# Kernel tuning notes

Hardware: AMD Instinct MI355X
Metric: run time of the kernel (lower is better)

Reference implementation:

```python
import jax, jax.numpy as jnp
import numpy as np

N_NODES = 50000
N_EDGES = 800000
IN_F = 256
OUT_F = 64
N_HEADS = 8
LRELU_SLOPE = 0.2


def setup_inputs() -> dict:
    key = jax.random.key(0)
    ks = jax.random.split(key, 6)
    x = jax.random.normal(ks[0], (N_NODES, IN_F), dtype=jnp.float32)
    src = jax.random.randint(ks[1], (N_EDGES,), 0, N_NODES, dtype=jnp.int32)
    dst = jax.random.randint(ks[2], (N_EDGES,), 0, N_NODES, dtype=jnp.int32)
    M_values = jax.random.uniform(ks[3], (N_EDGES,), dtype=jnp.float32)
    # xavier_uniform-ish scale (gain=1.414)
    wscale = 1.414 * np.sqrt(6.0 / (IN_F + OUT_F))
    W = jax.random.uniform(ks[4], (N_HEADS, IN_F, OUT_F), dtype=jnp.float32,
                           minval=-wscale, maxval=wscale)
    ascale = 1.414 * np.sqrt(6.0 / (OUT_F + 1))
    a = jax.random.uniform(ks[5], (N_HEADS, 2, OUT_F), dtype=jnp.float32,
                           minval=-ascale, maxval=ascale)
    return {"x": x, "src": src, "dst": dst, "M_values": M_values, "W": W, "a": a}


def reference(x, src, dst, M_values, W, a):
    # x: [N, Fin]; src/dst: [E]; M_values: [E] (edge-aligned mask/weights)
    # W: [H, Fin, Fout]; a: [H, 2, Fout] (a[:,0]=a_self, a[:,1]=a_neighs)
    N = x.shape[0]
    outs = []
    for hidx in range(W.shape[0]):  # small fixed head count
        h = x @ W[hidx]                       # [N, Fout]
        a_self = h @ a[hidx, 0]               # [N]
        a_neigh = h @ a[hidx, 1]              # [N]
        e = jax.nn.leaky_relu(a_self[src] + a_neigh[dst], LRELU_SLOPE) * M_values  # [E]
        exp_e = jnp.exp(e)
        denom = jax.ops.segment_sum(exp_e, dst, num_segments=N)   # [N]
        att = exp_e / (denom[dst] + 1e-16)                        # [E]
        h_prime = jax.ops.segment_sum(att[:, None] * h[src], dst, num_segments=N)  # [N, Fout]
        outs.append(jax.nn.elu(h_prime))      # concat=True -> elu per head
    return jnp.concatenate(outs, axis=1)       # [N, H*Fout]
```

## Files before the change

### kernel.cpp

```cpp
#include <hip/hip_runtime.h>
#include <math.h>

#define N_NODES 50000
#define N_EDGES 800000
#define IN_F 256
#define OUT_F 64
#define N_HEADS 8
#define SLOPE 0.2f

typedef __attribute__((ext_vector_type(8))) __bf16 bf16x8;
typedef __attribute__((ext_vector_type(4))) __bf16 bf16x4;
typedef __attribute__((ext_vector_type(4))) float floatx4;
typedef __attribute__((ext_vector_type(4))) float f32x4;
typedef __attribute__((ext_vector_type(2))) int i32x2;
typedef __attribute__((ext_vector_type(8))) char schar8;

#define HIST_BLOCKS   3125
#define CAST_W_BLOCKS 512
#define PREP_BLOCKS   (HIST_BLOCKS + CAST_W_BLOCKS)

__global__ __launch_bounds__(256) void prep_kernel(const float* __restrict__ W,
                                                   const int* __restrict__ dst,
                                                   __bf16* __restrict__ Wt,
                                                   int* __restrict__ deg) {
    const int b = blockIdx.x;
    const int t = threadIdx.x;
    if (b < HIST_BLOCKS) {
        int e = b * 256 + t;
        atomicAdd(&deg[dst[e]], 1);
    } else {
        int i = (b - HIST_BLOCKS) * 256 + t;
        int n = i & (OUT_F - 1);
        int k = (i >> 6) & (IN_F - 1);
        int h = i >> 14;
        Wt[((size_t)h * OUT_F + n) * IN_F + k] = (__bf16)W[i];
    }
}

#define XPAD 264
__global__ __launch_bounds__(256) void mfma_gemm_kernel(const float* __restrict__ x,
                                                        const __bf16* __restrict__ Wt,
                                                        const float* __restrict__ a,
                                                        signed char* __restrict__ hb,
                                                        float2* __restrict__ asc,
                                                        float* __restrict__ a_neigh) {
    __shared__ __bf16 xs[32][XPAD];
    const int warp = threadIdx.x >> 6;
    const int tile = blockIdx.x;
    const int n0 = tile * 32;
    const int lane = threadIdx.x & 63;
    const int l15 = lane & 15;
    const int quad = lane >> 4;
    const int h0 = warp * 2;

#pragma unroll
    for (int i = 0; i < 8; i++) {
        int c4 = i * 256 + threadIdx.x;
        int row = c4 >> 6;
        int col = (c4 & 63) * 4;
        int node = n0 + row;
        node = (node < N_NODES) ? node : (N_NODES - 1);
        f32x4 v = __builtin_nontemporal_load((const f32x4*)x + (size_t)node * 64 + (c4 & 63));
        bf16x4 o;
        o[0] = (__bf16)v[0]; o[1] = (__bf16)v[1]; o[2] = (__bf16)v[2]; o[3] = (__bf16)v[3];
        *(bf16x4*)&xs[row][col] = o;
    }
    __syncthreads();

    floatx4 acc[2][2][4];
#pragma unroll
    for (int hh = 0; hh < 2; hh++)
#pragma unroll
        for (int i = 0; i < 2; i++)
#pragma unroll
            for (int c = 0; c < 4; c++) acc[hh][i][c] = floatx4{0.f, 0.f, 0.f, 0.f};

    const __bf16* wb0 = Wt + ((size_t)h0 * OUT_F + l15) * IN_F + quad * 8;
    const __bf16* wb1 = wb0 + (size_t)OUT_F * IN_F;

#pragma unroll
    for (int k0 = 0; k0 < IN_F; k0 += 32) {
        bf16x8 a0 = *(const bf16x8*)&xs[l15][k0 + quad * 8];
        bf16x8 a1 = *(const bf16x8*)&xs[l15 + 16][k0 + quad * 8];
#pragma unroll
        for (int c = 0; c < 4; c++) {
            bf16x8 b0 = *(const bf16x8*)(wb0 + (size_t)c * 16 * IN_F + k0);
            acc[0][0][c] = __builtin_amdgcn_mfma_f32_16x16x32_bf16(a0, b0, acc[0][0][c], 0, 0, 0);
            acc[0][1][c] = __builtin_amdgcn_mfma_f32_16x16x32_bf16(a1, b0, acc[0][1][c], 0, 0, 0);
            bf16x8 b1 = *(const bf16x8*)(wb1 + (size_t)c * 16 * IN_F + k0);
            acc[1][0][c] = __builtin_amdgcn_mfma_f32_16x16x32_bf16(a0, b1, acc[1][0][c], 0, 0, 0);
            acc[1][1][c] = __builtin_amdgcn_mfma_f32_16x16x32_bf16(a1, b1, acc[1][1][c], 0, 0, 0);
        }
    }

    __syncthreads();
    char* myc = (char*)xs + warp * (32 * OUT_F);

#pragma unroll
    for (int hh = 0; hh < 2; hh++) {
        const int head = h0 + hh;
        float av0[4], av1[4];
#pragma unroll
        for (int c = 0; c < 4; c++) {
            av0[c] = a[head * 2 * OUT_F + c * 16 + l15];
            av1[c] = a[head * 2 * OUT_F + OUT_F + c * 16 + l15];
        }
#pragma unroll
        for (int i = 0; i < 2; i++) {
#pragma unroll
            for (int reg = 0; reg < 4; reg++) {
                float ps = 0.f, pn = 0.f, rm = 0.f;
#pragma unroll
                for (int c = 0; c < 4; c++) {
                    float v = acc[hh][i][c][reg];
                    ps = fmaf(v, av0[c], ps);
                    pn = fmaf(v, av1[c], pn);
                    rm = fmaxf(rm, fabsf(v));
                }
#pragma unroll
                for (int off = 1; off < 16; off <<= 1) {
                    ps += __shfl_xor(ps, off, 64);
                    pn += __shfl_xor(pn, off, 64);
                    rm = fmaxf(rm, __shfl_xor(rm, off, 64));
                }
                const float inv = (rm > 0.f) ? 127.f / rm : 0.f;
                const int rowoff = (i * 16 + quad * 4 + reg) * OUT_F;
#pragma unroll
                for (int c = 0; c < 4; c++) {
                    float q = rintf(acc[hh][i][c][reg] * inv);
                    q = fminf(fmaxf(q, -127.f), 127.f);
                    myc[rowoff + c * 16 + l15] = (char)(int)q;
                }
                int node = n0 + i * 16 + quad * 4 + reg;
                if (l15 == 0 && node < N_NODES) {
                    asc[node * N_HEADS + head] = make_float2(ps, rm * (1.f / 127.f));
                    a_neigh[node * N_HEADS + head] = pn;
                }
            }
        }
#pragma unroll
        for (int pass = 0; pass < 4; pass++) {
            int row = pass * 8 + (lane >> 3);
            int node = n0 + row;
            schar8 v = *(const schar8*)&myc[row * OUT_F + (lane & 7) * 8];
            if (node < N_NODES)
                *(schar8*)(hb + ((size_t)(node * N_HEADS + head) << 6) + (lane & 7) * 8) = v;
        }
    }
}

#define SB 512
#define NSB 98
__global__ void scanA(const int* __restrict__ deg, int* __restrict__ start,
                      int* __restrict__ bsum) {
    __shared__ int tmp[SB];
    int t = threadIdx.x, i = blockIdx.x * SB + t;
    int v = (i < N_NODES) ? deg[i] : 0;
    tmp[t] = v;
    for (int off = 1; off < SB; off <<= 1) {
        __syncthreads();
        int add = (t >= off) ? tmp[t - off] : 0;
        __syncthreads();
        tmp[t] += add;
    }
    if (i < N_NODES) start[i] = tmp[t] - v;
    if (t == SB - 1) bsum[blockIdx.x] = tmp[SB - 1];
}

__global__ void scanC(int* __restrict__ start, const int* __restrict__ bsum,
                      int* __restrict__ cursor) {
    __shared__ int pre[128];
    int t = threadIdx.x;
    if (t < 128) pre[t] = (t < NSB) ? bsum[t] : 0;
    __syncthreads();
    for (int off = 1; off < 128; off <<= 1) {
        int add = (t < 128 && t >= off) ? pre[t - off] : 0;
        __syncthreads();
        if (t < 128) pre[t] += add;
        __syncthreads();
    }
    int excl = (blockIdx.x == 0) ? 0 : pre[blockIdx.x - 1];
    int i = blockIdx.x * SB + t;
    if (i < N_NODES) {
        int s = start[i] + excl;
        start[i] = s;
        cursor[i] = s;
    }
}

__global__ void fill_kernel(const int* __restrict__ src, const int* __restrict__ dst,
                            const float* __restrict__ M, int* __restrict__ cursor,
                            i32x2* __restrict__ csr_sm) {
    int e = blockIdx.x * 256 + threadIdx.x;
    if (e < N_EDGES) {
        int d = dst[e];
        int pos = atomicAdd(&cursor[d], 1);
        i32x2 v;
        v.x = src[e];
        v.y = __float_as_int(M[e]);
        __builtin_nontemporal_store(v, csr_sm + pos);
    }
}

__global__ __launch_bounds__(256) void agg_kernel(const signed char* __restrict__ hb,
                                                  const float2* __restrict__ asc,
                                                  const float* __restrict__ a_neigh,
                                                  const int* __restrict__ start,
                                                  const int* __restrict__ deg,
                                                  const i32x2* __restrict__ csr_sm,
                                                  float* __restrict__ out) {
    int n = blockIdx.x * 4 + (threadIdx.x >> 6);
    if (n >= N_NODES) return;
    const int lane = threadIdx.x & 63;
    const int head = lane >> 3;

    const int d = deg[n];
    const float an = a_neigh[(n << 3) + head];
    const signed char* hbl = hb + (lane << 3);
    const float2* aslc = asc + head;
    const i32x2* cp = csr_sm + start[n];

    float facc[8];
#pragma unroll
    for (int k = 0; k < 8; k++) facc[k] = 0.f;
    float den = 0.f;

    i32x2 zero = 0;
    i32x2 smA = (d > 0) ? cp[0] : zero;
    i32x2 smB = (d > 1) ? cp[1] : smA;
    i32x2 smC = (d > 2) ? cp[2] : smB;
    i32x2 smD = (d > 3) ? cp[3] : smC;
    float2 aA = aslc[(size_t)smA.x << 3];
    schar8 hvA = *(const schar8*)(hbl + ((size_t)smA.x << 9));
    float2 aB = aslc[(size_t)smB.x << 3];
    schar8 hvB = *(const schar8*)(hbl + ((size_t)smB.x << 9));

    int j = 0;
    for (; j + 2 <= d; j += 2) {
        i32x2 smE = (j + 4 < d) ? cp[j + 4] : smD;
        i32x2 smF = (j + 5 < d) ? cp[j + 5] : smE;
        float2 aC = aslc[(size_t)smC.x << 3];
        schar8 hvC = *(const schar8*)(hbl + ((size_t)smC.x << 9));
        float2 aD = aslc[(size_t)smD.x << 3];
        schar8 hvD = *(const schar8*)(hbl + ((size_t)smD.x << 9));

        float eA = aA.x + an;
        eA = (eA > 0.f) ? eA : SLOPE * eA;
        const float wA = __expf(eA * __int_as_float(smA.y));
        const float wsA = wA * aA.y;
#pragma unroll
        for (int k = 0; k < 8; k++) facc[k] = fmaf(wsA, (float)hvA[k], facc[k]);
        den += wA;

        float eB = aB.x + an;
        eB = (eB > 0.f) ? eB : SLOPE * eB;
        const float wB = __expf(eB * __int_as_float(smB.y));
        const float wsB = wB * aB.y;
#pragma unroll
        for (int k = 0; k < 8; k++) facc[k] = fmaf(wsB, (float)hvB[k], facc[k]);
        den += wB;

        smA = smC; aA = aC; hvA = hvC;
        smB = smD; aB = aD; hvB = hvD;
        smC = smE; smD = smF;
    }
    if (j < d) {
        float eA = aA.x + an;
        eA = (eA > 0.f) ? eA : SLOPE * eA;
        const float wA = __expf(eA * __int_as_float(smA.y));
        const float wsA = wA * aA.y;
#pragma unroll
        for (int k = 0; k < 8; k++) facc[k] = fmaf(wsA, (float)hvA[k], facc[k]);
        den += wA;
    }

    const float inv = 1.f / (den + 1e-16f);
    float r[8];
#pragma unroll
    for (int k = 0; k < 8; k++) {
        float v = facc[k] * inv;
        r[k] = (v > 0.f) ? v : expm1f(v);
    }
    float* ob = &out[((size_t)n << 9) + (lane << 3)];
    *(float4*)(ob)     = make_float4(r[0], r[1], r[2], r[3]);
    *(float4*)(ob + 4) = make_float4(r[4], r[5], r[6], r[7]);
}

extern "C" void kernel_launch(void* const* d_in, const int* in_sizes, int n_in,
                              void* d_out, int out_size, void* d_ws, size_t ws_size,
                              hipStream_t stream) {
    const float* x   = (const float*)d_in[0];
    const int*   src = (const int*)d_in[1];
    const int*   dst = (const int*)d_in[2];
    const float* M   = (const float*)d_in[3];
    const float* W   = (const float*)d_in[4];
    const float* a   = (const float*)d_in[5];
    float* out = (float*)d_out;

    char* p = (char*)d_ws;
    auto alloc = [&](size_t bytes) {
        char* r = p;
        p += (bytes + 255) & ~(size_t)255;
        return r;
    };
    signed char* hb = (signed char*)alloc((size_t)N_NODES * N_HEADS * OUT_F);
    float2* asc     = (float2*)alloc(sizeof(float2) * N_NODES * N_HEADS);
    float*  a_neigh = (float*)alloc(sizeof(float) * N_NODES * N_HEADS);
    int*    deg     = (int*)alloc(sizeof(int) * N_NODES);
    int*    start   = (int*)alloc(sizeof(int) * N_NODES);
    int*    cursor  = (int*)alloc(sizeof(int) * N_NODES);
    int*    bsum    = (int*)alloc(sizeof(int) * 256);
    i32x2*  csr_sm  = (i32x2*)alloc(sizeof(i32x2) * N_EDGES);
    __bf16* Wt      = (__bf16*)alloc(sizeof(__bf16) * N_HEADS * IN_F * OUT_F);

    hipMemsetAsync(deg, 0, sizeof(int) * N_NODES, stream);
    prep_kernel<<<PREP_BLOCKS, 256, 0, stream>>>(W, dst, Wt, deg);

    scanA<<<NSB, SB, 0, stream>>>(deg, start, bsum);
    scanC<<<NSB, SB, 0, stream>>>(start, bsum, cursor);
    fill_kernel<<<(N_EDGES + 255) / 256, 256, 0, stream>>>(src, dst, M, cursor, csr_sm);

    mfma_gemm_kernel<<<1563, 256, 0, stream>>>(x, Wt, a, hb, asc, a_neigh);

    agg_kernel<<<(N_NODES + 3) / 4, 256, 0, stream>>>(hb, asc, a_neigh,
                                                      start, deg, csr_sm, out);
}
```

Baseline: 404.6 us.

## Use offset-unsigned int8 features, exp2 with prescaled mask, shallower prefetch in aggregation

Stores quantized features as unsigned bytes offset by 128 so the aggregation can unpack them with shifts and masks and convert unsigned integers to float. The 128 offset is subtracted once at the end using a running sum of the weights. The mask is prescaled by log2(e) in the CSR fill so the kernel can call exp2f instead of expf. The software pipeline is cut from four edges in flight to two, and zero-degree nodes exit early. The shallower prefetch lowers register use but can expose more gather latency, and the offset subtraction may add rounding error.

```diff
diff --git a/kernel.cpp b/kernel.cpp
--- a/kernel.cpp
+++ b/kernel.cpp
@@ -13,6 +13,7 @@
 typedef __attribute__((ext_vector_type(4))) float floatx4;
 typedef __attribute__((ext_vector_type(4))) float f32x4;
 typedef __attribute__((ext_vector_type(2))) int i32x2;
+typedef __attribute__((ext_vector_type(2))) unsigned int u32x2;
 typedef __attribute__((ext_vector_type(8))) char schar8;
 
 #define HIST_BLOCKS   3125
@@ -41,7 +42,7 @@
 __global__ __launch_bounds__(256) void mfma_gemm_kernel(const float* __restrict__ x,
                                                         const __bf16* __restrict__ Wt,
                                                         const float* __restrict__ a,
-                                                        signed char* __restrict__ hb,
+                                                        unsigned char* __restrict__ hb,
                                                         float2* __restrict__ asc,
                                                         float* __restrict__ a_neigh) {
     __shared__ __bf16 xs[32][XPAD];
@@ -129,7 +130,7 @@
                 for (int c = 0; c < 4; c++) {
                     float q = rintf(acc[hh][i][c][reg] * inv);
                     q = fminf(fmaxf(q, -127.f), 127.f);
-                    myc[rowoff + c * 16 + l15] = (char)(int)q;
+                    myc[rowoff + c * 16 + l15] = (char)((int)q + 128);
                 }
                 int node = n0 + i * 16 + quad * 4 + reg;
                 if (l15 == 0 && node < N_NODES) {
@@ -197,12 +198,12 @@
         int pos = atomicAdd(&cursor[d], 1);
         i32x2 v;
         v.x = src[e];
-        v.y = __float_as_int(M[e]);
+        v.y = __float_as_int(M[e] * 1.44269504f);
         __builtin_nontemporal_store(v, csr_sm + pos);
     }
 }
 
-__global__ __launch_bounds__(256) void agg_kernel(const signed char* __restrict__ hb,
+__global__ __launch_bounds__(256) void agg_kernel(const unsigned char* __restrict__ hb,
                                                   const float2* __restrict__ asc,
                                                   const float* __restrict__ a_neigh,
                                                   const int* __restrict__ start,
@@ -215,73 +216,66 @@
     const int head = lane >> 3;
 
     const int d = deg[n];
+    float* ob = &out[((size_t)n << 9) + (lane << 3)];
+    if (d == 0) {
+        f32x4 z = {0.f, 0.f, 0.f, 0.f};
+        *(f32x4*)(ob) = z;
+        *(f32x4*)(ob + 4) = z;
+        return;
+    }
+    const int dm1 = d - 1;
     const float an = a_neigh[(n << 3) + head];
-    const signed char* hbl = hb + (lane << 3);
+    const unsigned char* hbl = hb + (lane << 3);
     const float2* aslc = asc + head;
     const i32x2* cp = csr_sm + start[n];
 
     float facc[8];
 #pragma unroll
     for (int k = 0; k < 8; k++) facc[k] = 0.f;
-    float den = 0.f;
-
-    i32x2 zero = 0;
-    i32x2 smA = (d > 0) ? cp[0] : zero;
-    i32x2 smB = (d > 1) ? cp[1] : smA;
-    i32x2 smC = (d > 2) ? cp[2] : smB;
-    i32x2 smD = (d > 3) ? cp[3] : smC;
-    float2 aA = aslc[(size_t)smA.x << 3];
-    schar8 hvA = *(const schar8*)(hbl + ((size_t)smA.x << 9));
-    float2 aB = aslc[(size_t)smB.x << 3];
-    schar8 hvB = *(const schar8*)(hbl + ((size_t)smB.x << 9));
+    float den = 0.f, sacc = 0.f;
+
+    auto edge = [&](const i32x2& sm, const float2& a2, const u32x2& hv) {
+        float e_ = a2.x + an;
+        e_ = (e_ > 0.f) ? e_ : SLOPE * e_;
+        const float w_ = exp2f(e_ * __int_as_float(sm.y));
+        const float ws = w_ * a2.y;
+        den += w_;
+        sacc += ws;
+        facc[0] = fmaf(ws, (float)(hv.x & 0xffu), facc[0]);
+        facc[1] = fmaf(ws, (float)((hv.x >> 8) & 0xffu), facc[1]);
+        facc[2] = fmaf(ws, (float)((hv.x >> 16) & 0xffu), facc[2]);
+        facc[3] = fmaf(ws, (float)(hv.x >> 24), facc[3]);
+        facc[4] = fmaf(ws, (float)(hv.y & 0xffu), facc[4]);
+        facc[5] = fmaf(ws, (float)((hv.y >> 8) & 0xffu), facc[5]);
+        facc[6] = fmaf(ws, (float)((hv.y >> 16) & 0xffu), facc[6]);
+        facc[7] = fmaf(ws, (float)(hv.y >> 24), facc[7]);
+    };
+
+    i32x2 smP = cp[0];
+    float2 aP = aslc[(size_t)smP.x << 3];
+    u32x2 hvP = *(const u32x2*)(hbl + ((size_t)smP.x << 9));
 
     int j = 0;
     for (; j + 2 <= d; j += 2) {
-        i32x2 smE = (j + 4 < d) ? cp[j + 4] : smD;
-        i32x2 smF = (j + 5 < d) ? cp[j + 5] : smE;
-        float2 aC = aslc[(size_t)smC.x << 3];
-        schar8 hvC = *(const schar8*)(hbl + ((size_t)smC.x << 9));
-        float2 aD = aslc[(size_t)smD.x << 3];
-        schar8 hvD = *(const schar8*)(hbl + ((size_t)smD.x << 9));
-
-        float eA = aA.x + an;
-        eA = (eA > 0.f) ? eA : SLOPE * eA;
-        const float wA = __expf(eA * __int_as_float(smA.y));
-        const float wsA = wA * aA.y;
-#pragma unroll
-        for (int k = 0; k < 8; k++) facc[k] = fmaf(wsA, (float)hvA[k], facc[k]);
-        den += wA;
-
-        float eB = aB.x + an;
-        eB = (eB > 0.f) ? eB : SLOPE * eB;
-        const float wB = __expf(eB * __int_as_float(smB.y));
-        const float wsB = wB * aB.y;
-#pragma unroll
-        for (int k = 0; k < 8; k++) facc[k] = fmaf(wsB, (float)hvB[k], facc[k]);
-        den += wB;
-
-        smA = smC; aA = aC; hvA = hvC;
-        smB = smD; aB = aD; hvB = hvD;
-        smC = smE; smD = smF;
-    }
-    if (j < d) {
-        float eA = aA.x + an;
-        eA = (eA > 0.f) ? eA : SLOPE * eA;
-        const float wA = __expf(eA * __int_as_float(smA.y));
-        const float wsA = wA * aA.y;
-#pragma unroll
-        for (int k = 0; k < 8; k++) facc[k] = fmaf(wsA, (float)hvA[k], facc[k]);
-        den += wA;
-    }
+        i32x2 smQ = cp[j + 1];
+        float2 aQ = aslc[(size_t)smQ.x << 3];
+        u32x2 hvQ = *(const u32x2*)(hbl + ((size_t)smQ.x << 9));
+        edge(smP, aP, hvP);
+        int i2 = (j + 2 < d) ? (j + 2) : dm1;
+        smP = cp[i2];
+        aP = aslc[(size_t)smP.x << 3];
+        hvP = *(const u32x2*)(hbl + ((size_t)smP.x << 9));
+        edge(smQ, aQ, hvQ);
+    }
+    if (j < d) edge(smP, aP, hvP);
 
     const float inv = 1.f / (den + 1e-16f);
     float r[8];
 #pragma unroll
     for (int k = 0; k < 8; k++) {
-        float v = facc[k] * inv;
+        float v = fmaf(-128.f, sacc, facc[k]) * inv;
         r[k] = (v > 0.f) ? v : expm1f(v);
     }
-    float* ob = &out[((size_t)n << 9) + (lane << 3)];
     *(float4*)(ob)     = make_float4(r[0], r[1], r[2], r[3]);
     *(float4*)(ob + 4) = make_float4(r[4], r[5], r[6], r[7]);
 }
@@ -303,7 +297,7 @@
         p += (bytes + 255) & ~(size_t)255;
         return r;
     };
-    signed char* hb = (signed char*)alloc((size_t)N_NODES * N_HEADS * OUT_F);
+    unsigned char* hb = (unsigned char*)alloc((size_t)N_NODES * N_HEADS * OUT_F);
     float2* asc     = (float2*)alloc(sizeof(float2) * N_NODES * N_HEADS);
     float*  a_neigh = (float*)alloc(sizeof(float) * N_NODES * N_HEADS);
     int*    deg     = (int*)alloc(sizeof(int) * N_NODES);
```

Result: no change. 401.3 us (-0.8%).
